# Kernel tuning notes

Measured on AMD Instinct MI355X. Metric: run time of the kernel, lower is better.

## Reference

```python
import jax, jax.numpy as jnp
import numpy as np

N = 20000   # mesh vertices
B = 8       # batch
F = 64      # in_channels
K = 6       # Chebyshev order
OUT = 64    # out_channels
NNZ = 320000  # nonzeros in sparse Laplacian (avg degree 16)


def setup_inputs() -> dict:
    key = jax.random.key(0)
    ks = jax.random.split(key, 6)
    x = jax.random.normal(ks[0], (B, N, F), dtype=jnp.float32)
    lap_rows = jax.random.randint(ks[1], (NNZ,), 0, N, dtype=jnp.int32)
    lap_cols = jax.random.randint(ks[2], (NNZ,), 0, N, dtype=jnp.int32)
    lap_vals = jax.random.normal(ks[3], (NNZ,), dtype=jnp.float32) * 0.05
    # fc: Linear(K*F, OUT), xavier_normal weight, zero bias
    W = jax.random.normal(ks[4], (OUT, K * F), dtype=jnp.float32) * float(np.sqrt(2.0 / (K * F + OUT)))
    b = jnp.zeros((OUT,), dtype=jnp.float32)
    return {"x": x, "lap_rows": lap_rows, "lap_cols": lap_cols,
            "lap_vals": lap_vals, "W": W, "b": b}


def reference(x, lap_rows, lap_cols, lap_vals, W, b):
    Bd, Nd, Fd = x.shape

    def spmm(v):  # sparse [N,N] @ dense [N, B*F] via COO gather + segment_sum
        return jax.ops.segment_sum(lap_vals[:, None] * v[lap_cols], lap_rows,
                                   num_segments=Nd)

    x0 = jnp.transpose(x, (1, 0, 2)).reshape(Nd, Bd * Fd)  # [N, B*F]
    outs = [x0]
    if K > 1:
        tx1 = spmm(x0)
        outs.append(tx1)
        tx0 = x0
        for _ in range(2, K):  # Chebyshev recurrence T_k = 2 L T_{k-1} - T_{k-2}
            tx2 = 2.0 * spmm(tx1) - tx0
            outs.append(tx2)
            tx0, tx1 = tx1, tx2
    out = jnp.concatenate([o.reshape(Nd, Bd, Fd) for o in outs], axis=2)  # [N,B,K*F]
    out = out.reshape(Nd * Bd, K * Fd) @ W.T + b  # dense fc
    return jnp.transpose(out.reshape(Nd, Bd, -1), (1, 0, 2))  # [B,N,OUT]
```

## Files before the change

kernel.cpp:

```cpp
#include <hip/hip_runtime.h>

#define N_V  20000
#define B_   8
#define F_   64
#define K_   6
#define OUT_ 64
#define NNZ_ 320000
#define BF   512
#define NSLICE 8
#define SLICE_W 2500
#define NPAIR (N_V / 2)
#define NBUK (NPAIR * NSLICE)
#define SCANB 79

typedef unsigned short ushort_t;
typedef unsigned int   uint_t;

using frag_ab = __attribute__((ext_vector_type(8))) short;
using frag_cd = __attribute__((ext_vector_type(4))) float;

__device__ __forceinline__ ushort_t f2bf(float f) {
    uint_t u = __float_as_uint(f);
    u += 0x7FFFu + ((u >> 16) & 1u);
    return (ushort_t)(u >> 16);
}
__device__ __forceinline__ uint_t pack2(float lo, float hi) {
    return (uint_t)f2bf(lo) | ((uint_t)f2bf(hi) << 16);
}
__device__ __forceinline__ void unpack2(uint_t u, float& lo, float& hi) {
    lo = __uint_as_float(u << 16);
    hi = __uint_as_float(u & 0xFFFF0000u);
}


__global__ void hist_kernel(const int* __restrict__ rows, const int* __restrict__ cols,
                            int* __restrict__ counts) {
    int e = blockIdx.x * 256 + threadIdx.x;
    if (e < NNZ_) {
        int key = (rows[e] >> 1) * NSLICE + cols[e] / SLICE_W;
        atomicAdd(&counts[key], 1);
    }
}

__global__ __launch_bounds__(1024) void scan1(const int* __restrict__ counts,
                                              int* __restrict__ incl, int* __restrict__ bsum) {
    __shared__ int buf[1024];
    int tid = threadIdx.x;
    int i = blockIdx.x * 1024 + tid;
    int c = (i < NBUK) ? counts[i] : 0;
    buf[tid] = c;
    __syncthreads();
    for (int off = 1; off < 1024; off <<= 1) {
        int t = buf[tid];
        int add = (tid >= off) ? buf[tid - off] : 0;
        __syncthreads();
        buf[tid] = t + add;
        __syncthreads();
    }
    if (i < NBUK) incl[i] = buf[tid];
    if (tid == 1023) bsum[blockIdx.x] = buf[1023];
}

__global__ __launch_bounds__(256) void scan2(int* __restrict__ bsum) {
    __shared__ int buf[256];
    int tid = threadIdx.x;
    int c = (tid < SCANB) ? bsum[tid] : 0;
    buf[tid] = c;
    __syncthreads();
    for (int off = 1; off < 256; off <<= 1) {
        int t = buf[tid];
        int add = (tid >= off) ? buf[tid - off] : 0;
        __syncthreads();
        buf[tid] = t + add;
        __syncthreads();
    }
    if (tid < SCANB) bsum[tid] = buf[tid] - c;
}

__global__ __launch_bounds__(1024) void scan3(const int* __restrict__ counts,
                                              const int* __restrict__ bsum,
                                              int* __restrict__ bp, int* __restrict__ cursor) {
    int tid = threadIdx.x;
    int i = blockIdx.x * 1024 + tid;
    if (i < NBUK) {
        int p = bsum[blockIdx.x] + cursor[i];
        bp[i + 1] = p;
        cursor[i] = p - counts[i];
    }
    if (i == 0) bp[0] = 0;
}

__global__ void scatter_kernel(const int* __restrict__ rows, const int* __restrict__ cols,
                               const float* __restrict__ vals, int* __restrict__ cursor,
                               int2* __restrict__ edges) {
    int e = blockIdx.x * 256 + threadIdx.x;
    if (e < NNZ_) {
        int c = cols[e];
        int r = rows[e];
        int key = (r >> 1) * NSLICE + c / SLICE_W;
        int pos = atomicAdd(&cursor[key], 1);
        int2 pe;
        pe.x = c | ((r & 1) << 15);
        pe.y = __float_as_int(vals[e]);
        edges[pos] = pe;
    }
}

__global__ void prep_kernel(const float* __restrict__ x, uint_t* __restrict__ X0,
                            const float* __restrict__ W, ushort_t* __restrict__ Wfrag) {
    int blk = blockIdx.x;
    if (blk < 20000) {
        int idx = blk * 256 + threadIdx.x;
        int f2 = idx & 31;
        int b  = (idx >> 5) & 7;
        int n  = idx >> 8;
        float2 v = *(const float2*)&x[((size_t)b * N_V + n) * F_ + f2 * 2];
        X0[n * 256 + b * 32 + f2] = pack2(v.x, v.y);
    } else {
        int idx = (blk - 20000) * 256 + threadIdx.x;
        if (idx < 12 * 4 * 64 * 8) {
            int j    = idx & 7;
            int lane = (idx >> 3) & 63;
            int ct   = (idx >> 9) & 3;
            int s    = idx >> 11;
            int o     = ct * 16 + (lane & 15);
            int kglob = s * 32 + ((lane >> 4) & 3) * 8 + j;
            Wfrag[idx] = f2bf(W[o * (K_ * F_) + kglob]);
        }
    }
}

template <bool RECUR>
__global__ __launch_bounds__(256) void cheb_pair(const int* __restrict__ bp,
                                                 const int2* __restrict__ edges,
                                                 const ushort_t* __restrict__ Tprev,
                                                 const ushort_t* __restrict__ Tpp,
                                                 ushort_t* __restrict__ Tout) {
    const int wave = threadIdx.x >> 6, lane = threadIdx.x & 63;
    const int pair = blockIdx.x * 4 + wave;
    const int n0 = pair * 2;
    const int fo = lane * 8;
    const int st = bp[pair * NSLICE];
    const int en = bp[pair * NSLICE + NSLICE];

    float a0[8], a1[8];
#pragma unroll
    for (int i = 0; i < 8; ++i) { a0[i] = 0.f; a1[i] = 0.f; }

    for (int j = st; j < en; j += 8) {
        int2 E[8];
#pragma unroll
        for (int q = 0; q < 8; ++q) {
            E[q] = edges[min(j + q, en - 1)];
        }
        uint4 u[8];
#pragma unroll
        for (int q = 0; q < 8; ++q) {
            u[q] = *(const uint4*)(Tprev + (size_t)(E[q].x & 0x7FFF) * BF + fo);
        }
#pragma unroll
        for (int q = 0; q < 8; ++q) {
            const float v  = (j + q < en) ? __int_as_float(E[q].y) : 0.f;
            const float p0 = (E[q].x & 0x8000) ? 0.f : v;
            const float p1 = (E[q].x & 0x8000) ? v : 0.f;
            float e[8];
            unpack2(u[q].x, e[0], e[1]); unpack2(u[q].y, e[2], e[3]);
            unpack2(u[q].z, e[4], e[5]); unpack2(u[q].w, e[6], e[7]);
#pragma unroll
            for (int i = 0; i < 8; ++i) {
                a0[i] = fmaf(p0, e[i], a0[i]);
                a1[i] = fmaf(p1, e[i], a1[i]);
            }
        }
    }

    {
        float res[8];
#pragma unroll
        for (int i = 0; i < 8; ++i) res[i] = a0[i];
        if (RECUR) {
            uint4 up = *(const uint4*)(Tpp + (size_t)n0 * BF + fo);
            float ep[8];
            unpack2(up.x, ep[0], ep[1]); unpack2(up.y, ep[2], ep[3]);
            unpack2(up.z, ep[4], ep[5]); unpack2(up.w, ep[6], ep[7]);
#pragma unroll
            for (int i = 0; i < 8; ++i) res[i] = 2.f * res[i] - ep[i];
        }
        uint4 st4;
        st4.x = pack2(res[0], res[1]);
        st4.y = pack2(res[2], res[3]);
        st4.z = pack2(res[4], res[5]);
        st4.w = pack2(res[6], res[7]);
        *(uint4*)(Tout + (size_t)n0 * BF + fo) = st4;
    }
    {
        float res[8];
#pragma unroll
        for (int i = 0; i < 8; ++i) res[i] = a1[i];
        if (RECUR) {
            uint4 up = *(const uint4*)(Tpp + (size_t)(n0 + 1) * BF + fo);
            float ep[8];
            unpack2(up.x, ep[0], ep[1]); unpack2(up.y, ep[2], ep[3]);
            unpack2(up.z, ep[4], ep[5]); unpack2(up.w, ep[6], ep[7]);
#pragma unroll
            for (int i = 0; i < 8; ++i) res[i] = 2.f * res[i] - ep[i];
        }
        uint4 st4;
        st4.x = pack2(res[0], res[1]);
        st4.y = pack2(res[2], res[3]);
        st4.z = pack2(res[4], res[5]);
        st4.w = pack2(res[6], res[7]);
        *(uint4*)(Tout + (size_t)(n0 + 1) * BF + fo) = st4;
    }
}

__global__ __launch_bounds__(256) void fc_mfma(const ushort_t* __restrict__ X0,
                                               const ushort_t* __restrict__ T1,
                                               const ushort_t* __restrict__ T2,
                                               const ushort_t* __restrict__ T3,
                                               const ushort_t* __restrict__ T4,
                                               const ushort_t* __restrict__ T5,
                                               const ushort_t* __restrict__ Wfrag,
                                               const float* __restrict__ bias,
                                               float* __restrict__ out) {
    const int wave = threadIdx.x >> 6, lane = threadIdx.x & 63;
    const int quad = lane >> 4, col = lane & 15;
    const int tb = blockIdx.x * 128 + wave * 32;
    const int r0 = tb + col, r1 = tb + 16 + col;
    const ushort_t* Tbuf[6] = {X0, T1, T2, T3, T4, T5};

    frag_cd acc0[4], acc1[4];
#pragma unroll
    for (int ct = 0; ct < 4; ++ct) {
        acc0[ct] = (frag_cd){0.f, 0.f, 0.f, 0.f};
        acc1[ct] = (frag_cd){0.f, 0.f, 0.f, 0.f};
    }

#pragma unroll
    for (int s = 0; s < 12; ++s) {
        const int f0 = (s & 1) * 32 + quad * 8;
        frag_ab fa0 = *(const frag_ab*)(Tbuf[s >> 1] + (size_t)r0 * F_ + f0);
        frag_ab fa1 = *(const frag_ab*)(Tbuf[s >> 1] + (size_t)r1 * F_ + f0);
#pragma unroll
        for (int ct = 0; ct < 4; ++ct) {
            frag_ab bfr = *(const frag_ab*)(Wfrag + (((s * 4 + ct) * 64 + lane) << 3));
            acc0[ct] = __builtin_amdgcn_mfma_f32_16x16x32_bf16(fa0, bfr, acc0[ct], 0, 0, 0);
            acc1[ct] = __builtin_amdgcn_mfma_f32_16x16x32_bf16(fa1, bfr, acc1[ct], 0, 0, 0);
        }
    }

#pragma unroll
    for (int ct = 0; ct < 4; ++ct) {
        const int o = ct * 16 + col;
        const float bv = bias[o];
#pragma unroll
        for (int reg = 0; reg < 4; ++reg) {
            int ra = tb + quad * 4 + reg;
            int rb = ra + 16;
            out[(size_t)(ra & 7) * N_V * OUT_ + (size_t)(ra >> 3) * OUT_ + o] = acc0[ct][reg] + bv;
            out[(size_t)(rb & 7) * N_V * OUT_ + (size_t)(rb >> 3) * OUT_ + o] = acc1[ct][reg] + bv;
        }
    }
}


extern "C" void kernel_launch(void* const* d_in, const int* in_sizes, int n_in,
                              void* d_out, int out_size, void* d_ws, size_t ws_size,
                              hipStream_t stream) {
    const float* x    = (const float*)d_in[0];
    const int*   rows = (const int*)  d_in[1];
    const int*   cols = (const int*)  d_in[2];
    const float* vals = (const float*)d_in[3];
    const float* W    = (const float*)d_in[4];
    const float* bias = (const float*)d_in[5];
    float* out = (float*)d_out;

    const size_t TSZ = (size_t)N_V * BF;
    ushort_t* T1 = (ushort_t*)d_ws;
    ushort_t* T2 = T1 + TSZ;
    ushort_t* T3 = T2 + TSZ;
    ushort_t* T4 = T3 + TSZ;
    ushort_t* T5 = T4 + TSZ;
    ushort_t* X0 = T5 + TSZ;
    ushort_t* Wfrag = X0 + TSZ;
    int* counts    = (int*)(Wfrag + 24576);
    int* bp        = counts + NBUK;
    int* cursor    = bp + NBUK + 64;
    int* bsum      = cursor + NBUK;
    int2* edges    = (int2*)(bsum + 256);

    hipMemsetAsync(counts, 0, NBUK * sizeof(int), stream);
    hist_kernel<<<(NNZ_ + 255) / 256, 256, 0, stream>>>(rows, cols, counts);
    scan1<<<SCANB, 1024, 0, stream>>>(counts, cursor, bsum);
    scan2<<<1, 256, 0, stream>>>(bsum);
    scan3<<<SCANB, 1024, 0, stream>>>(counts, bsum, bp, cursor);
    scatter_kernel<<<(NNZ_ + 255) / 256, 256, 0, stream>>>(rows, cols, vals, cursor, edges);
    prep_kernel<<<20096, 256, 0, stream>>>(x, (uint_t*)X0, W, Wfrag);

    cheb_pair<false><<<NPAIR / 4, 256, 0, stream>>>(bp, edges, X0, nullptr, T1);
    cheb_pair<true ><<<NPAIR / 4, 256, 0, stream>>>(bp, edges, T1, X0, T2);
    cheb_pair<true ><<<NPAIR / 4, 256, 0, stream>>>(bp, edges, T2, T1, T3);
    cheb_pair<true ><<<NPAIR / 4, 256, 0, stream>>>(bp, edges, T3, T2, T4);
    cheb_pair<true ><<<NPAIR / 4, 256, 0, stream>>>(bp, edges, T4, T3, T5);

    fc_mfma<<<(N_V * B_) / 128, 256, 0, stream>>>(X0, T1, T2, T3, T4, T5, Wfrag, bias, out);
}
```

Measured before the change: 388.3 us.

## Switch SpMM to per-row CSR with padded edges and column-split waves

Replaces the row-pair, column-sliced bucketing with plain per-row CSR whose segments are padded to multiples of 8 with zeroed edges, which removes the bounds clamping and the per-edge row-parity selects. Each wave now handles one row and a 64-column slice of the 512 features, with the grid split 8 ways over columns. Edge indices and values are made wave-uniform through readfirstlane, and each lane gathers a single bf16 element per edge. The trade is 8x more blocks, each re-reading the row's edge list, narrow 2-byte gathers in place of 16-byte vector loads, and an extra memset of the padded edge buffer.

```diff
diff --git a/kernel.cpp b/kernel.cpp
--- a/kernel.cpp
+++ b/kernel.cpp
@@ -7,11 +7,9 @@
 #define OUT_ 64
 #define NNZ_ 320000
 #define BF   512
-#define NSLICE 8
-#define SLICE_W 2500
-#define NPAIR (N_V / 2)
-#define NBUK (NPAIR * NSLICE)
-#define SCANB 79
+#define NBUK N_V
+#define SCANB 20
+#define EPAD (NNZ_ + N_V * 7)
 
 typedef unsigned short ushort_t;
 typedef unsigned int   uint_t;
@@ -27,19 +25,14 @@
 __device__ __forceinline__ uint_t pack2(float lo, float hi) {
     return (uint_t)f2bf(lo) | ((uint_t)f2bf(hi) << 16);
 }
-__device__ __forceinline__ void unpack2(uint_t u, float& lo, float& hi) {
-    lo = __uint_as_float(u << 16);
-    hi = __uint_as_float(u & 0xFFFF0000u);
-}
-
-
-__global__ void hist_kernel(const int* __restrict__ rows, const int* __restrict__ cols,
-                            int* __restrict__ counts) {
+__device__ __forceinline__ float bf2f(ushort_t u) {
+    return __uint_as_float((uint_t)u << 16);
+}
+
+
+__global__ void hist_kernel(const int* __restrict__ rows, int* __restrict__ counts) {
     int e = blockIdx.x * 256 + threadIdx.x;
-    if (e < NNZ_) {
-        int key = (rows[e] >> 1) * NSLICE + cols[e] / SLICE_W;
-        atomicAdd(&counts[key], 1);
-    }
+    if (e < NNZ_) atomicAdd(&counts[rows[e]], 1);
 }
 
 __global__ __launch_bounds__(1024) void scan1(const int* __restrict__ counts,
@@ -47,7 +40,7 @@
     __shared__ int buf[1024];
     int tid = threadIdx.x;
     int i = blockIdx.x * 1024 + tid;
-    int c = (i < NBUK) ? counts[i] : 0;
+    int c = (i < NBUK) ? ((counts[i] + 7) & ~7) : 0;
     buf[tid] = c;
     __syncthreads();
     for (int off = 1; off < 1024; off <<= 1) {
@@ -83,9 +76,10 @@
     int tid = threadIdx.x;
     int i = blockIdx.x * 1024 + tid;
     if (i < NBUK) {
+        int pc = (counts[i] + 7) & ~7;
         int p = bsum[blockIdx.x] + cursor[i];
         bp[i + 1] = p;
-        cursor[i] = p - counts[i];
+        cursor[i] = p - pc;
     }
     if (i == 0) bp[0] = 0;
 }
@@ -95,14 +89,8 @@
                                int2* __restrict__ edges) {
     int e = blockIdx.x * 256 + threadIdx.x;
     if (e < NNZ_) {
-        int c = cols[e];
-        int r = rows[e];
-        int key = (r >> 1) * NSLICE + c / SLICE_W;
-        int pos = atomicAdd(&cursor[key], 1);
-        int2 pe;
-        pe.x = c | ((r & 1) << 15);
-        pe.y = __float_as_int(vals[e]);
-        edges[pos] = pe;
+        int pos = atomicAdd(&cursor[rows[e]], 1);
+        edges[pos] = make_int2(cols[e], __float_as_int(vals[e]));
     }
 }
 
@@ -131,87 +119,66 @@
 }
 
 template <bool RECUR>
-__global__ __launch_bounds__(256) void cheb_pair(const int* __restrict__ bp,
-                                                 const int2* __restrict__ edges,
-                                                 const ushort_t* __restrict__ Tprev,
-                                                 const ushort_t* __restrict__ Tpp,
-                                                 ushort_t* __restrict__ Tout) {
-    const int wave = threadIdx.x >> 6, lane = threadIdx.x & 63;
-    const int pair = blockIdx.x * 4 + wave;
-    const int n0 = pair * 2;
-    const int fo = lane * 8;
-    const int st = bp[pair * NSLICE];
-    const int en = bp[pair * NSLICE + NSLICE];
-
-    float a0[8], a1[8];
-#pragma unroll
-    for (int i = 0; i < 8; ++i) { a0[i] = 0.f; a1[i] = 0.f; }
-
+__global__ __launch_bounds__(256) void cheb_row(const int* __restrict__ bp,
+                                                const int2* __restrict__ edges,
+                                                const ushort_t* __restrict__ Tprev,
+                                                const ushort_t* __restrict__ Tpp,
+                                                ushort_t* __restrict__ Tout) {
+    const int wave = __builtin_amdgcn_readfirstlane(threadIdx.x >> 6);
+    const int lane = threadIdx.x & 63;
+    const int c    = blockIdx.x & 7;
+    const int row  = ((blockIdx.x >> 3) << 2) + wave;
+
+    const int st = bp[row];
+    const int en = bp[row + 1];
+    const ushort_t* Tp = Tprev + (c << 6) + lane;
+
+    float a0 = 0.f, a1 = 0.f;
     for (int j = st; j < en; j += 8) {
-        int2 E[8];
-#pragma unroll
-        for (int q = 0; q < 8; ++q) {
-            E[q] = edges[min(j + q, en - 1)];
-        }
-        uint4 u[8];
-#pragma unroll
-        for (int q = 0; q < 8; ++q) {
-            u[q] = *(const uint4*)(Tprev + (size_t)(E[q].x & 0x7FFF) * BF + fo);
-        }
-#pragma unroll
-        for (int q = 0; q < 8; ++q) {
-            const float v  = (j + q < en) ? __int_as_float(E[q].y) : 0.f;
-            const float p0 = (E[q].x & 0x8000) ? 0.f : v;
-            const float p1 = (E[q].x & 0x8000) ? v : 0.f;
-            float e[8];
-            unpack2(u[q].x, e[0], e[1]); unpack2(u[q].y, e[2], e[3]);
-            unpack2(u[q].z, e[4], e[5]); unpack2(u[q].w, e[6], e[7]);
-#pragma unroll
-            for (int i = 0; i < 8; ++i) {
-                a0[i] = fmaf(p0, e[i], a0[i]);
-                a1[i] = fmaf(p1, e[i], a1[i]);
-            }
-        }
-    }
-
-    {
-        float res[8];
-#pragma unroll
-        for (int i = 0; i < 8; ++i) res[i] = a0[i];
-        if (RECUR) {
-            uint4 up = *(const uint4*)(Tpp + (size_t)n0 * BF + fo);
-            float ep[8];
-            unpack2(up.x, ep[0], ep[1]); unpack2(up.y, ep[2], ep[3]);
-            unpack2(up.z, ep[4], ep[5]); unpack2(up.w, ep[6], ep[7]);
-#pragma unroll
-            for (int i = 0; i < 8; ++i) res[i] = 2.f * res[i] - ep[i];
-        }
-        uint4 st4;
-        st4.x = pack2(res[0], res[1]);
-        st4.y = pack2(res[2], res[3]);
-        st4.z = pack2(res[4], res[5]);
-        st4.w = pack2(res[6], res[7]);
-        *(uint4*)(Tout + (size_t)n0 * BF + fo) = st4;
-    }
-    {
-        float res[8];
-#pragma unroll
-        for (int i = 0; i < 8; ++i) res[i] = a1[i];
-        if (RECUR) {
-            uint4 up = *(const uint4*)(Tpp + (size_t)(n0 + 1) * BF + fo);
-            float ep[8];
-            unpack2(up.x, ep[0], ep[1]); unpack2(up.y, ep[2], ep[3]);
-            unpack2(up.z, ep[4], ep[5]); unpack2(up.w, ep[6], ep[7]);
-#pragma unroll
-            for (int i = 0; i < 8; ++i) res[i] = 2.f * res[i] - ep[i];
-        }
-        uint4 st4;
-        st4.x = pack2(res[0], res[1]);
-        st4.y = pack2(res[2], res[3]);
-        st4.z = pack2(res[4], res[5]);
-        st4.w = pack2(res[6], res[7]);
-        *(uint4*)(Tout + (size_t)(n0 + 1) * BF + fo) = st4;
-    }
+        const int4* e4 = (const int4*)(edges + j);
+        int4 E0 = e4[0], E1 = e4[1], E2 = e4[2], E3 = e4[3];
+        const int c0 = __builtin_amdgcn_readfirstlane(E0.x);
+        const int c1 = __builtin_amdgcn_readfirstlane(E0.z);
+        const int c2 = __builtin_amdgcn_readfirstlane(E1.x);
+        const int c3 = __builtin_amdgcn_readfirstlane(E1.z);
+        const int c4 = __builtin_amdgcn_readfirstlane(E2.x);
+        const int c5 = __builtin_amdgcn_readfirstlane(E2.z);
+        const int c6 = __builtin_amdgcn_readfirstlane(E3.x);
+        const int c7 = __builtin_amdgcn_readfirstlane(E3.z);
+        const float v0 = __int_as_float(__builtin_amdgcn_readfirstlane(E0.y));
+        const float v1 = __int_as_float(__builtin_amdgcn_readfirstlane(E0.w));
+        const float v2 = __int_as_float(__builtin_amdgcn_readfirstlane(E1.y));
+        const float v3 = __int_as_float(__builtin_amdgcn_readfirstlane(E1.w));
+        const float v4 = __int_as_float(__builtin_amdgcn_readfirstlane(E2.y));
+        const float v5 = __int_as_float(__builtin_amdgcn_readfirstlane(E2.w));
+        const float v6 = __int_as_float(__builtin_amdgcn_readfirstlane(E3.y));
+        const float v7 = __int_as_float(__builtin_amdgcn_readfirstlane(E3.w));
+
+        ushort_t t0 = Tp[(size_t)c0 << 9];
+        ushort_t t1 = Tp[(size_t)c1 << 9];
+        ushort_t t2 = Tp[(size_t)c2 << 9];
+        ushort_t t3 = Tp[(size_t)c3 << 9];
+        ushort_t t4 = Tp[(size_t)c4 << 9];
+        ushort_t t5 = Tp[(size_t)c5 << 9];
+        ushort_t t6 = Tp[(size_t)c6 << 9];
+        ushort_t t7 = Tp[(size_t)c7 << 9];
+
+        a0 = fmaf(v0, bf2f(t0), a0);
+        a1 = fmaf(v1, bf2f(t1), a1);
+        a0 = fmaf(v2, bf2f(t2), a0);
+        a1 = fmaf(v3, bf2f(t3), a1);
+        a0 = fmaf(v4, bf2f(t4), a0);
+        a1 = fmaf(v5, bf2f(t5), a1);
+        a0 = fmaf(v6, bf2f(t6), a0);
+        a1 = fmaf(v7, bf2f(t7), a1);
+    }
+
+    float res = a0 + a1;
+    const size_t oidx = (size_t)row * BF + (c << 6) + lane;
+    if (RECUR) {
+        res = fmaf(2.f, res, -bf2f(Tpp[oidx]));
+    }
+    Tout[oidx] = f2bf(res);
 }
 
 __global__ __launch_bounds__(256) void fc_mfma(const ushort_t* __restrict__ X0,
@@ -290,18 +257,20 @@
     int2* edges    = (int2*)(bsum + 256);
 
     hipMemsetAsync(counts, 0, NBUK * sizeof(int), stream);
-    hist_kernel<<<(NNZ_ + 255) / 256, 256, 0, stream>>>(rows, cols, counts);
+    hipMemsetAsync(edges, 0, (size_t)EPAD * sizeof(int2), stream);
+    hist_kernel<<<(NNZ_ + 255) / 256, 256, 0, stream>>>(rows, counts);
     scan1<<<SCANB, 1024, 0, stream>>>(counts, cursor, bsum);
     scan2<<<1, 256, 0, stream>>>(bsum);
     scan3<<<SCANB, 1024, 0, stream>>>(counts, bsum, bp, cursor);
     scatter_kernel<<<(NNZ_ + 255) / 256, 256, 0, stream>>>(rows, cols, vals, cursor, edges);
     prep_kernel<<<20096, 256, 0, stream>>>(x, (uint_t*)X0, W, Wfrag);
 
-    cheb_pair<false><<<NPAIR / 4, 256, 0, stream>>>(bp, edges, X0, nullptr, T1);
-    cheb_pair<true ><<<NPAIR / 4, 256, 0, stream>>>(bp, edges, T1, X0, T2);
-    cheb_pair<true ><<<NPAIR / 4, 256, 0, stream>>>(bp, edges, T2, T1, T3);
-    cheb_pair<true ><<<NPAIR / 4, 256, 0, stream>>>(bp, edges, T3, T2, T4);
-    cheb_pair<true ><<<NPAIR / 4, 256, 0, stream>>>(bp, edges, T4, T3, T5);
+    const int chebGrid = (N_V / 4) * 8;
+    cheb_row<false><<<chebGrid, 256, 0, stream>>>(bp, edges, X0, nullptr, T1);
+    cheb_row<true ><<<chebGrid, 256, 0, stream>>>(bp, edges, T1, X0, T2);
+    cheb_row<true ><<<chebGrid, 256, 0, stream>>>(bp, edges, T2, T1, T3);
+    cheb_row<true ><<<chebGrid, 256, 0, stream>>>(bp, edges, T3, T2, T4);
+    cheb_row<true ><<<chebGrid, 256, 0, stream>>>(bp, edges, T4, T3, T5);
 
     fc_mfma<<<(N_V * B_) / 128, 256, 0, stream>>>(X0, T1, T2, T3, T4, T5, Wfrag, bias, out);
 }
```

Result: slower. 453.0 us (+16.7%).

## Fuse histogram into prep, single-block scan, and persistent grid-stride cheb waves

Applied to the files above, without the earlier changes.

Merges the edge histogram into the x/W preparation kernel, replaces the three-kernel scan with one 1024-thread block where each thread serially scans 79 buckets, and makes cheb_pair a grid-stride loop over 8192 waves instead of one wave per vertex pair. The aim is fewer kernel launches and less launch or tail overhead in the preprocessing and SpMM stages. The single-block scan is serial per thread with strided, uncoalesced reads, and the grid-stride launch gives uneven wave counts, with some waves taking two pairs.

```diff
diff --git a/kernel.cpp b/kernel.cpp
--- a/kernel.cpp
+++ b/kernel.cpp
@@ -11,7 +11,7 @@
 #define SLICE_W 2500
 #define NPAIR (N_V / 2)
 #define NBUK (NPAIR * NSLICE)
-#define SCANB 79
+#define CHEB_WAVES 8192
 
 typedef unsigned short ushort_t;
 typedef unsigned int   uint_t;
@@ -32,23 +32,50 @@
     hi = __uint_as_float(u & 0xFFFF0000u);
 }
 
-
-__global__ void hist_kernel(const int* __restrict__ rows, const int* __restrict__ cols,
-                            int* __restrict__ counts) {
-    int e = blockIdx.x * 256 + threadIdx.x;
-    if (e < NNZ_) {
-        int key = (rows[e] >> 1) * NSLICE + cols[e] / SLICE_W;
-        atomicAdd(&counts[key], 1);
-    }
-}
-
-__global__ __launch_bounds__(1024) void scan1(const int* __restrict__ counts,
-                                              int* __restrict__ incl, int* __restrict__ bsum) {
+__global__ void prep_hist(const float* __restrict__ x, uint_t* __restrict__ X0,
+                          const float* __restrict__ W, ushort_t* __restrict__ Wfrag,
+                          const int* __restrict__ rows, const int* __restrict__ cols,
+                          int* __restrict__ counts) {
+    int blk = blockIdx.x;
+    if (blk < 20000) {
+        int idx = blk * 256 + threadIdx.x;
+        int f2 = idx & 31;
+        int b  = (idx >> 5) & 7;
+        int n  = idx >> 8;
+        float2 v = *(const float2*)&x[((size_t)b * N_V + n) * F_ + f2 * 2];
+        X0[n * 256 + b * 32 + f2] = pack2(v.x, v.y);
+    } else if (blk < 20096) {
+        int idx = (blk - 20000) * 256 + threadIdx.x;
+        if (idx < 12 * 4 * 64 * 8) {
+            int j    = idx & 7;
+            int lane = (idx >> 3) & 63;
+            int ct   = (idx >> 9) & 3;
+            int s    = idx >> 11;
+            int o     = ct * 16 + (lane & 15);
+            int kglob = s * 32 + ((lane >> 4) & 3) * 8 + j;
+            Wfrag[idx] = f2bf(W[o * (K_ * F_) + kglob]);
+        }
+    } else {
+        int e = (blk - 20096) * 256 + threadIdx.x;
+        if (e < NNZ_) {
+            int key = (rows[e] >> 1) * NSLICE + cols[e] / SLICE_W;
+            atomicAdd(&counts[key], 1);
+        }
+    }
+}
+
+__global__ __launch_bounds__(1024) void scan80k(const int* __restrict__ counts,
+                                                int* __restrict__ bp,
+                                                int* __restrict__ cursor) {
     __shared__ int buf[1024];
-    int tid = threadIdx.x;
-    int i = blockIdx.x * 1024 + tid;
-    int c = (i < NBUK) ? counts[i] : 0;
-    buf[tid] = c;
+    const int tid = threadIdx.x;
+    const int base = tid * 79;
+    int s = 0;
+    for (int k = 0; k < 79; ++k) {
+        int i = base + k;
+        if (i < NBUK) s += counts[i];
+    }
+    buf[tid] = s;
     __syncthreads();
     for (int off = 1; off < 1024; off <<= 1) {
         int t = buf[tid];
@@ -57,37 +84,16 @@
         buf[tid] = t + add;
         __syncthreads();
     }
-    if (i < NBUK) incl[i] = buf[tid];
-    if (tid == 1023) bsum[blockIdx.x] = buf[1023];
-}
-
-__global__ __launch_bounds__(256) void scan2(int* __restrict__ bsum) {
-    __shared__ int buf[256];
-    int tid = threadIdx.x;
-    int c = (tid < SCANB) ? bsum[tid] : 0;
-    buf[tid] = c;
-    __syncthreads();
-    for (int off = 1; off < 256; off <<= 1) {
-        int t = buf[tid];
-        int add = (tid >= off) ? buf[tid - off] : 0;
-        __syncthreads();
-        buf[tid] = t + add;
-        __syncthreads();
-    }
-    if (tid < SCANB) bsum[tid] = buf[tid] - c;
-}
-
-__global__ __launch_bounds__(1024) void scan3(const int* __restrict__ counts,
-                                              const int* __restrict__ bsum,
-                                              int* __restrict__ bp, int* __restrict__ cursor) {
-    int tid = threadIdx.x;
-    int i = blockIdx.x * 1024 + tid;
-    if (i < NBUK) {
-        int p = bsum[blockIdx.x] + cursor[i];
-        bp[i + 1] = p;
-        cursor[i] = p - counts[i];
-    }
-    if (i == 0) bp[0] = 0;
+    int run = buf[tid] - s;
+    for (int k = 0; k < 79; ++k) {
+        int i = base + k;
+        if (i < NBUK) {
+            bp[i] = run;
+            cursor[i] = run;
+            run += counts[i];
+        }
+    }
+    if (tid == 1023) bp[NBUK] = buf[1023];
 }
 
 __global__ void scatter_kernel(const int* __restrict__ rows, const int* __restrict__ cols,
@@ -106,30 +112,6 @@
     }
 }
 
-__global__ void prep_kernel(const float* __restrict__ x, uint_t* __restrict__ X0,
-                            const float* __restrict__ W, ushort_t* __restrict__ Wfrag) {
-    int blk = blockIdx.x;
-    if (blk < 20000) {
-        int idx = blk * 256 + threadIdx.x;
-        int f2 = idx & 31;
-        int b  = (idx >> 5) & 7;
-        int n  = idx >> 8;
-        float2 v = *(const float2*)&x[((size_t)b * N_V + n) * F_ + f2 * 2];
-        X0[n * 256 + b * 32 + f2] = pack2(v.x, v.y);
-    } else {
-        int idx = (blk - 20000) * 256 + threadIdx.x;
-        if (idx < 12 * 4 * 64 * 8) {
-            int j    = idx & 7;
-            int lane = (idx >> 3) & 63;
-            int ct   = (idx >> 9) & 3;
-            int s    = idx >> 11;
-            int o     = ct * 16 + (lane & 15);
-            int kglob = s * 32 + ((lane >> 4) & 3) * 8 + j;
-            Wfrag[idx] = f2bf(W[o * (K_ * F_) + kglob]);
-        }
-    }
-}
-
 template <bool RECUR>
 __global__ __launch_bounds__(256) void cheb_pair(const int* __restrict__ bp,
                                                  const int2* __restrict__ edges,
@@ -137,80 +119,82 @@
                                                  const ushort_t* __restrict__ Tpp,
                                                  ushort_t* __restrict__ Tout) {
     const int wave = threadIdx.x >> 6, lane = threadIdx.x & 63;
-    const int pair = blockIdx.x * 4 + wave;
-    const int n0 = pair * 2;
     const int fo = lane * 8;
-    const int st = bp[pair * NSLICE];
-    const int en = bp[pair * NSLICE + NSLICE];
-
-    float a0[8], a1[8];
-#pragma unroll
-    for (int i = 0; i < 8; ++i) { a0[i] = 0.f; a1[i] = 0.f; }
-
-    for (int j = st; j < en; j += 8) {
-        int2 E[8];
-#pragma unroll
-        for (int q = 0; q < 8; ++q) {
-            E[q] = edges[min(j + q, en - 1)];
-        }
-        uint4 u[8];
-#pragma unroll
-        for (int q = 0; q < 8; ++q) {
-            u[q] = *(const uint4*)(Tprev + (size_t)(E[q].x & 0x7FFF) * BF + fo);
-        }
-#pragma unroll
-        for (int q = 0; q < 8; ++q) {
-            const float v  = (j + q < en) ? __int_as_float(E[q].y) : 0.f;
-            const float p0 = (E[q].x & 0x8000) ? 0.f : v;
-            const float p1 = (E[q].x & 0x8000) ? v : 0.f;
-            float e[8];
-            unpack2(u[q].x, e[0], e[1]); unpack2(u[q].y, e[2], e[3]);
-            unpack2(u[q].z, e[4], e[5]); unpack2(u[q].w, e[6], e[7]);
-#pragma unroll
-            for (int i = 0; i < 8; ++i) {
-                a0[i] = fmaf(p0, e[i], a0[i]);
-                a1[i] = fmaf(p1, e[i], a1[i]);
-            }
-        }
-    }
-
-    {
-        float res[8];
-#pragma unroll
-        for (int i = 0; i < 8; ++i) res[i] = a0[i];
-        if (RECUR) {
-            uint4 up = *(const uint4*)(Tpp + (size_t)n0 * BF + fo);
-            float ep[8];
-            unpack2(up.x, ep[0], ep[1]); unpack2(up.y, ep[2], ep[3]);
-            unpack2(up.z, ep[4], ep[5]); unpack2(up.w, ep[6], ep[7]);
-#pragma unroll
-            for (int i = 0; i < 8; ++i) res[i] = 2.f * res[i] - ep[i];
-        }
-        uint4 st4;
-        st4.x = pack2(res[0], res[1]);
-        st4.y = pack2(res[2], res[3]);
-        st4.z = pack2(res[4], res[5]);
-        st4.w = pack2(res[6], res[7]);
-        *(uint4*)(Tout + (size_t)n0 * BF + fo) = st4;
-    }
-    {
-        float res[8];
-#pragma unroll
-        for (int i = 0; i < 8; ++i) res[i] = a1[i];
-        if (RECUR) {
-            uint4 up = *(const uint4*)(Tpp + (size_t)(n0 + 1) * BF + fo);
-            float ep[8];
-            unpack2(up.x, ep[0], ep[1]); unpack2(up.y, ep[2], ep[3]);
-            unpack2(up.z, ep[4], ep[5]); unpack2(up.w, ep[6], ep[7]);
-#pragma unroll
-            for (int i = 0; i < 8; ++i) res[i] = 2.f * res[i] - ep[i];
-        }
-        uint4 st4;
-        st4.x = pack2(res[0], res[1]);
-        st4.y = pack2(res[2], res[3]);
-        st4.z = pack2(res[4], res[5]);
-        st4.w = pack2(res[6], res[7]);
-        *(uint4*)(Tout + (size_t)(n0 + 1) * BF + fo) = st4;
+
+    for (int pair = blockIdx.x * 4 + wave; pair < NPAIR; pair += CHEB_WAVES) {
+        const int n0 = pair * 2;
+        const int st = bp[pair * NSLICE];
+        const int en = bp[pair * NSLICE + NSLICE];
+
+        float a0[8], a1[8];
+#pragma unroll
+        for (int i = 0; i < 8; ++i) { a0[i] = 0.f; a1[i] = 0.f; }
+
+        for (int j = st; j < en; j += 8) {
+            int2 E[8];
+#pragma unroll
+            for (int q = 0; q < 8; ++q) {
+                E[q] = edges[min(j + q, en - 1)];
+            }
+            uint4 u[8];
+#pragma unroll
+            for (int q = 0; q < 8; ++q) {
+                u[q] = *(const uint4*)(Tprev + (size_t)(E[q].x & 0x7FFF) * BF + fo);
+            }
+#pragma unroll
+            for (int q = 0; q < 8; ++q) {
+                const float v  = (j + q < en) ? __int_as_float(E[q].y) : 0.f;
+                const float p0 = (E[q].x & 0x8000) ? 0.f : v;
+                const float p1 = (E[q].x & 0x8000) ? v : 0.f;
+                float e[8];
+                unpack2(u[q].x, e[0], e[1]); unpack2(u[q].y, e[2], e[3]);
+                unpack2(u[q].z, e[4], e[5]); unpack2(u[q].w, e[6], e[7]);
+#pragma unroll
+                for (int i = 0; i < 8; ++i) {
+                    a0[i] = fmaf(p0, e[i], a0[i]);
+                    a1[i] = fmaf(p1, e[i], a1[i]);
+                }
+            }
+        }
+
+        {
+            float res[8];
+#pragma unroll
+            for (int i = 0; i < 8; ++i) res[i] = a0[i];
+            if (RECUR) {
+                uint4 up = *(const uint4*)(Tpp + (size_t)n0 * BF + fo);
+                float ep[8];
+                unpack2(up.x, ep[0], ep[1]); unpack2(up.y, ep[2], ep[3]);
+                unpack2(up.z, ep[4], ep[5]); unpack2(up.w, ep[6], ep[7]);
+#pragma unroll
+                for (int i = 0; i < 8; ++i) res[i] = 2.f * res[i] - ep[i];
+            }
+            uint4 st4;
+            st4.x = pack2(res[0], res[1]);
+            st4.y = pack2(res[2], res[3]);
+            st4.z = pack2(res[4], res[5]);
+            st4.w = pack2(res[6], res[7]);
+            *(uint4*)(Tout + (size_t)n0 * BF + fo) = st4;
+        }
+        {
+            float res[8];
+#pragma unroll
+            for (int i = 0; i < 8; ++i) res[i] = a1[i];
+            if (RECUR) {
+                uint4 up = *(const uint4*)(Tpp + (size_t)(n0 + 1) * BF + fo);
+                float ep[8];
+                unpack2(up.x, ep[0], ep[1]); unpack2(up.y, ep[2], ep[3]);
+                unpack2(up.z, ep[4], ep[5]); unpack2(up.w, ep[6], ep[7]);
+#pragma unroll
+                for (int i = 0; i < 8; ++i) res[i] = 2.f * res[i] - ep[i];
+            }
+            uint4 st4;
+            st4.x = pack2(res[0], res[1]);
+            st4.y = pack2(res[2], res[3]);
+            st4.z = pack2(res[4], res[5]);
+            st4.w = pack2(res[6], res[7]);
+            *(uint4*)(Tout + (size_t)(n0 + 1) * BF + fo) = st4;
+        }
     }
 }
 
@@ -286,22 +270,18 @@
     int* counts    = (int*)(Wfrag + 24576);
     int* bp        = counts + NBUK;
     int* cursor    = bp + NBUK + 64;
-    int* bsum      = cursor + NBUK;
-    int2* edges    = (int2*)(bsum + 256);
+    int2* edges    = (int2*)(cursor + NBUK);
 
     hipMemsetAsync(counts, 0, NBUK * sizeof(int), stream);
-    hist_kernel<<<(NNZ_ + 255) / 256, 256, 0, stream>>>(rows, cols, counts);
-    scan1<<<SCANB, 1024, 0, stream>>>(counts, cursor, bsum);
-    scan2<<<1, 256, 0, stream>>>(bsum);
-    scan3<<<SCANB, 1024, 0, stream>>>(counts, bsum, bp, cursor);
+    prep_hist<<<20096 + 1250, 256, 0, stream>>>(x, (uint_t*)X0, W, Wfrag, rows, cols, counts);
+    scan80k<<<1, 1024, 0, stream>>>(counts, bp, cursor);
     scatter_kernel<<<(NNZ_ + 255) / 256, 256, 0, stream>>>(rows, cols, vals, cursor, edges);
-    prep_kernel<<<20096, 256, 0, stream>>>(x, (uint_t*)X0, W, Wfrag);
-
-    cheb_pair<false><<<NPAIR / 4, 256, 0, stream>>>(bp, edges, X0, nullptr, T1);
-    cheb_pair<true ><<<NPAIR / 4, 256, 0, stream>>>(bp, edges, T1, X0, T2);
-    cheb_pair<true ><<<NPAIR / 4, 256, 0, stream>>>(bp, edges, T2, T1, T3);
-    cheb_pair<true ><<<NPAIR / 4, 256, 0, stream>>>(bp, edges, T3, T2, T4);
-    cheb_pair<true ><<<NPAIR / 4, 256, 0, stream>>>(bp, edges, T4, T3, T5);
+
+    cheb_pair<false><<<CHEB_WAVES / 4, 256, 0, stream>>>(bp, edges, X0, nullptr, T1);
+    cheb_pair<true ><<<CHEB_WAVES / 4, 256, 0, stream>>>(bp, edges, T1, X0, T2);
+    cheb_pair<true ><<<CHEB_WAVES / 4, 256, 0, stream>>>(bp, edges, T2, T1, T3);
+    cheb_pair<true ><<<CHEB_WAVES / 4, 256, 0, stream>>>(bp, edges, T3, T2, T4);
+    cheb_pair<true ><<<CHEB_WAVES / 4, 256, 0, stream>>>(bp, edges, T4, T3, T5);
 
     fc_mfma<<<(N_V * B_) / 128, 256, 0, stream>>>(X0, T1, T2, T3, T4, T5, Wfrag, bias, out);
 }
```

After: 579.3 us. 1.49x slower.
